# Kernel optimization log

Measured on AMD Instinct MI355X. Metric: run time of the kernel, lower is better.

Reference implementation:

```python
import jax, jax.numpy as jnp
import numpy as np

BATCH = 1024
IN_DIM = 64
OUT_DIM = 64
K = 3          # spline order
G = 16         # internal intervals
G_LOW = 0.0
G_HIGH = 1.0
N_KNOTS = G + 2 * K + 1   # 23
N_COEF = G + K            # 19


def setup_inputs() -> dict:
    key = jax.random.key(0)
    kx, kc = jax.random.split(key)
    x = jax.random.uniform(kx, (BATCH, IN_DIM), dtype=jnp.float32)  # in [g_low, g_high)
    # Xavier-uniform-like init for coeff (out, in, G+k)
    limit = np.sqrt(6.0 / (IN_DIM * N_COEF + OUT_DIM * N_COEF)).astype(np.float32)
    coeff = jax.random.uniform(kc, (OUT_DIM, IN_DIM, N_COEF), dtype=jnp.float32,
                               minval=-limit, maxval=limit)
    # Extended uniform knot vector, replicated per (out, in) pair (buffer in torch)
    h = (G_HIGH - G_LOW) / G
    knots = jnp.linspace(G_LOW - K * h, G_HIGH + K * h, N_KNOTS, dtype=jnp.float32)
    grid = jnp.broadcast_to(knots, (OUT_DIM, IN_DIM, N_KNOTS))
    return {"x": x, "coeff": coeff, "grid": grid}


def _bspline_bases(x, grid, k):
    """Cox-de Boor recursion.
    x: (B, in); grid: (out, in, G+2k+1) -> bases: (B, out, in, G+k)."""
    xe = x[:, None, :, None]  # (B, 1, in, 1)
    # degree-0 indicator bases: (B, out, in, G+2k)
    bases = ((xe >= grid[..., :-1]) & (xe < grid[..., 1:])).astype(x.dtype)
    for p in range(1, k + 1):
        left = (xe - grid[..., : -(p + 1)]) / (grid[..., p:-1] - grid[..., : -(p + 1)])
        right = (grid[..., p + 1:] - xe) / (grid[..., p + 1:] - grid[..., 1:-p])
        bases = left * bases[..., :-1] + right * bases[..., 1:]
    return bases  # (B, out, in, G+k)


def reference(x, coeff, grid):
    bases = _bspline_bases(x, grid, K)                 # (B, out, in, G+k)
    # weighted sum over basis dim, faithful to torch: sum(bases * coeff[None], -1)
    return jnp.einsum('boig,oig->boi', bases, coeff)   # (B, out, in)
```

## Files before the change

kernel.cpp:

```cpp
#include <hip/hip_runtime.h>

#define BATCH   1024
#define IN_DIM  64
#define OUT_DIM 64
#define KORD    3
#define NKNOTS  23
#define NCOEF   19

__global__ __launch_bounds__(256) void spline_kernel(
    const float* __restrict__ x,
    const float* __restrict__ coeff,
    const float* __restrict__ grid,
    float* __restrict__ out)
{
    __shared__ float sN[IN_DIM][5];
    __shared__ int   sJ[IN_DIM];

    const int b = blockIdx.x;
    const int t = threadIdx.x;

    if (t < IN_DIM) {
        const int i = t;
        const float xv = x[b * IN_DIM + i];
        const float* tk = grid + i * NKNOTS;
        float kn[NKNOTS];
        #pragma unroll
        for (int m = 0; m < NKNOTS; ++m) kn[m] = tk[m];

        int j = -1;
        #pragma unroll
        for (int m = 0; m < NKNOTS - 1; ++m)
            if (xv >= kn[m] && xv < kn[m + 1]) j = m;

        float N[4] = {0.f, 0.f, 0.f, 0.f};
        int jj = 0;
        if (j >= 0) {
            if (j < KORD) j = KORD;
            if (j > NKNOTS - 2 - KORD) j = NKNOTS - 2 - KORD;
            N[0] = 1.f;
            #pragma unroll
            for (int p = 1; p <= KORD; ++p) {
                #pragma unroll
                for (int s = KORD; s >= 0; --s) {
                    if (s > p) continue;
                    const int m = j - p + s;
                    const float left  = (s >= 1)     ? N[s - 1] : 0.f;
                    const float right = (s <= p - 1) ? N[s]     : 0.f;
                    const float a = (xv - kn[m])         / (kn[m + p]     - kn[m]);
                    const float c = (kn[m + p + 1] - xv) / (kn[m + p + 1] - kn[m + 1]);
                    N[s] = a * left + c * right;
                }
            }
            jj = j - KORD;
        }
        sN[i][0] = N[0];
        sN[i][1] = N[1];
        sN[i][2] = N[2];
        sN[i][3] = N[3];
        sJ[i] = jj;
    }
    __syncthreads();

    const int i  = t & 63;
    const int og = t >> 6;
    const int jj = sJ[i];
    const float n0 = sN[i][0];
    const float n1 = sN[i][1];
    const float n2 = sN[i][2];
    const float n3 = sN[i][3];

    float* __restrict__ outb = out + (size_t)b * (OUT_DIM * IN_DIM);
    #pragma unroll
    for (int r = 0; r < 16; ++r) {
        const int o = og * 16 + r;
        const float* __restrict__ cp = coeff + ((size_t)o * IN_DIM + i) * NCOEF + jj;
        const float v = n0 * cp[0] + n1 * cp[1] + n2 * cp[2] + n3 * cp[3];
        outb[o * IN_DIM + i] = v;
    }
}

extern "C" void kernel_launch(void* const* d_in, const int* in_sizes, int n_in,
                              void* d_out, int out_size, void* d_ws, size_t ws_size,
                              hipStream_t stream) {
    const float* x     = (const float*)d_in[0];
    const float* coeff = (const float*)d_in[1];
    const float* grid  = (const float*)d_in[2];
    float* out = (float*)d_out;

    spline_kernel<<<BATCH, 256, 0, stream>>>(x, coeff, grid, out);
}
```

Baseline: 74.37 us.

## Tile over batch and output dims, staging coefficient tile in shared memory

Restructures the launch into a 2D grid of batch tiles (8 rows) by output tiles (8 outputs). Each block copies a contiguous 8x64x19 coefficient slice into LDS with float4 loads and computes basis values for 8 batch rows, then evaluates outputs from shared memory. The goal is to replace the strided, uncoalesced global coefficient gathers with LDS reads and reuse each coefficient tile across batch rows. In exchange, each block uses about 39KB of LDS, which lowers occupancy, and basis values are recomputed once per output tile.

Result: slower. 77.18 us (+3.8%).

```diff
diff --git a/kernel.cpp b/kernel.cpp
--- a/kernel.cpp
+++ b/kernel.cpp
@@ -6,6 +6,9 @@
 #define KORD    3
 #define NKNOTS  23
 #define NCOEF   19
+#define BT      8
+#define OT      8
+#define CTILE   (OT * IN_DIM * NCOEF)
 
 __global__ __launch_bounds__(256) void spline_kernel(
     const float* __restrict__ x,
@@ -13,16 +16,31 @@
     const float* __restrict__ grid,
     float* __restrict__ out)
 {
-    __shared__ float sN[IN_DIM][5];
-    __shared__ int   sJ[IN_DIM];
+    __shared__ __align__(16) float sC[CTILE];
+    __shared__ float sB[4][BT][IN_DIM];
+    __shared__ int   sJ[BT][IN_DIM];
 
-    const int b = blockIdx.x;
-    const int t = threadIdx.x;
+    const int t  = threadIdx.x;
+    const int bt = blockIdx.x;
+    const int ot = blockIdx.y;
 
-    if (t < IN_DIM) {
-        const int i = t;
-        const float xv = x[b * IN_DIM + i];
-        const float* tk = grid + i * NKNOTS;
+    {
+        const float4* __restrict__ src =
+            (const float4*)(coeff + (size_t)ot * CTILE);
+        float4* dst = (float4*)sC;
+        #pragma unroll
+        for (int idx = t; idx < CTILE / 4; idx += 256)
+            dst[idx] = src[idx];
+    }
+
+    #pragma unroll
+    for (int q = 0; q < (BT * IN_DIM) / 256; ++q) {
+        const int pair = t + q * 256;
+        const int i  = pair & 63;
+        const int lb = pair >> 6;
+        const float xv = x[(size_t)(bt * BT + lb) * IN_DIM + i];
+
+        const float* __restrict__ tk = grid + i * NKNOTS;
         float kn[NKNOTS];
         #pragma unroll
         for (int m = 0; m < NKNOTS; ++m) kn[m] = tk[m];
@@ -53,29 +71,27 @@
             }
             jj = j - KORD;
         }
-        sN[i][0] = N[0];
-        sN[i][1] = N[1];
-        sN[i][2] = N[2];
-        sN[i][3] = N[3];
-        sJ[i] = jj;
+        sB[0][lb][i] = N[0];
+        sB[1][lb][i] = N[1];
+        sB[2][lb][i] = N[2];
+        sB[3][lb][i] = N[3];
+        sJ[lb][i] = jj;
     }
     __syncthreads();
 
-    const int i  = t & 63;
-    const int og = t >> 6;
-    const int jj = sJ[i];
-    const float n0 = sN[i][0];
-    const float n1 = sN[i][1];
-    const float n2 = sN[i][2];
-    const float n3 = sN[i][3];
+    const int i   = t & 63;
+    const int sub = t >> 6;
 
-    float* __restrict__ outb = out + (size_t)b * (OUT_DIM * IN_DIM);
     #pragma unroll
     for (int r = 0; r < 16; ++r) {
-        const int o = og * 16 + r;
-        const float* __restrict__ cp = coeff + ((size_t)o * IN_DIM + i) * NCOEF + jj;
-        const float v = n0 * cp[0] + n1 * cp[1] + n2 * cp[2] + n3 * cp[3];
-        outb[o * IN_DIM + i] = v;
+        const int p  = sub + 4 * r;
+        const int lb = p & (BT - 1);
+        const int lo = p >> 3;
+        const int jj = sJ[lb][i];
+        const float* __restrict__ cp = &sC[(lo * IN_DIM + i) * NCOEF + jj];
+        const float v = sB[0][lb][i] * cp[0] + sB[1][lb][i] * cp[1]
+                      + sB[2][lb][i] * cp[2] + sB[3][lb][i] * cp[3];
+        out[((size_t)(bt * BT + lb) * OUT_DIM + (ot * OT + lo)) * IN_DIM + i] = v;
     }
 }
 
@@ -87,5 +103,6 @@
     const float* grid  = (const float*)d_in[2];
     float* out = (float*)d_out;
 
-    spline_kernel<<<BATCH, 256, 0, stream>>>(x, coeff, grid, out);
+    dim3 g(BATCH / BT, OUT_DIM / OT);
+    spline_kernel<<<g, 256, 0, stream>>>(x, coeff, grid, out);
 }
```
